# Kernel optimization log

Hardware: AMD Instinct MI355X
Metric: run time of the kernel (lower is better)

Reference implementation:

```python
import jax, jax.numpy as jnp
import numpy as np


def setup_inputs() -> dict:
    key = jax.random.key(0)
    k1, k2, k3 = jax.random.split(key, 3)
    x = jax.random.normal(k1, (8192, 2048), dtype=jnp.float32)
    w = jax.random.normal(k2, (4096, 2048), dtype=jnp.float32) * 0.02  # [out, in]
    b = jax.random.normal(k3, (4096,), dtype=jnp.float32) * 0.01
    return {"x": x, "w": w, "b": b}


def reference(x, w, b):
    # Straight-through binarization: forward uses sign(w), gradient flows as identity.
    binary_w = w + jax.lax.stop_gradient(jnp.sign(w) - w)  # [out, in], values in {-1, 0, 1}
    # F.linear: x @ W^T + b
    return jnp.einsum("ni,oi->no", x, binary_w) + b
```

## Files before the change

kernel.cpp:

```cpp
#include <hip/hip_runtime.h>
#include <hip/hip_bf16.h>
#include <stdint.h>

typedef __bf16 bf16x8 __attribute__((ext_vector_type(8)));
typedef float  f32x16 __attribute__((ext_vector_type(16)));


__device__ __forceinline__ uint32_t rn2_bf16(uint32_t lo, uint32_t hi) {
  uint32_t rlo = (lo + 0x7FFFu + ((lo >> 16) & 1u)) >> 16;
  uint32_t rhi = (hi + 0x7FFFu + ((hi >> 16) & 1u)) >> 16;
  return (rhi << 16) | (rlo & 0xFFFFu);
}

__device__ __forceinline__ uint32_t sign2_bf16(uint32_t lo, uint32_t hi) {
  uint32_t slo = (lo & 0x7FFFFFFFu) ? (0x3F80u | ((lo >> 16) & 0x8000u)) : 0u;
  uint32_t shi = (hi & 0x7FFFFFFFu) ? (0x3F80u | ((hi >> 16) & 0x8000u)) : 0u;
  return (shi << 16) | slo;
}

__device__ __forceinline__ void gl16(const void* g, void* l) {
  __builtin_amdgcn_global_load_lds(
      (const __attribute__((address_space(1))) uint32_t*)g,
      (__attribute__((address_space(3))) uint32_t*)l,
      16, 0, 0);
}


__global__ void prep_frag(const float* __restrict__ x, uint4* __restrict__ xf, int Mx,
                          const float* __restrict__ w, uint4* __restrict__ wf, int Nw,
                          int K) {
  const int kpw = K >> 6;
  const long nxc = ((long)Mx * K) >> 3;
  const long nwc = ((long)Nw * K) >> 3;
  const long stride = (long)gridDim.x * blockDim.x;
  for (long c = (long)blockIdx.x * blockDim.x + threadIdx.x; c < nxc + nwc; c += stride) {
    const bool isX = (c < nxc);
    const float* src = isX ? x : w;
    uint4* dst = isX ? xf : wf;
    const int rows32 = (isX ? Mx : Nw) >> 5;
    const long cc = isX ? c : (c - nxc);

    const int t = (int)(cc & 63);
    const long wv = cc >> 6;
    const int band = (int)(wv / kpw);
    const int kg = (int)(wv % kpw);
    const int row = band * 8 + (t & 7);
    const int k8 = kg * 8 + (t >> 3);

    const int kt = k8 >> 3, ks = (k8 >> 1) & 3, sub = k8 & 1;
    const int mb = row >> 5, r = row & 31;
    const long out16 = ((long)(kt * rows32 + mb) * 4 + ks) * 64 + sub * 32 + r;

    const uint4* s = reinterpret_cast<const uint4*>(src + (long)row * K + k8 * 8);
    uint4 a = s[0], b = s[1];
    uint4 o;
    if (isX) {
      o.x = rn2_bf16(a.x, a.y); o.y = rn2_bf16(a.z, a.w);
      o.z = rn2_bf16(b.x, b.y); o.w = rn2_bf16(b.z, b.w);
    } else {
      o.x = sign2_bf16(a.x, a.y); o.y = sign2_bf16(a.z, a.w);
      o.z = sign2_bf16(b.x, b.y); o.w = sign2_bf16(b.z, b.w);
    }
    dst[out16] = o;
  }
}


#define BARX()  do { __builtin_amdgcn_s_barrier(); \
                     __builtin_amdgcn_sched_barrier(0); } while (0)
#define VM0()   asm volatile("s_waitcnt vmcnt(0)" ::: "memory")
#define VMN8()  asm volatile("s_waitcnt vmcnt(8)" ::: "memory")
#define SGB(m, n) __builtin_amdgcn_sched_group_barrier((m), (n), 0)
#define MF(a, b, c) __builtin_amdgcn_mfma_f32_32x32x16_bf16((a), (b), (c), 0, 0, 0)

#define PIN6() do { \
    SGB(0x100,1); SGB(0x8,1); SGB(0x100,1); SGB(0x8,1); \
    SGB(0x100,1); SGB(0x8,1); SGB(0x100,1); SGB(0x8,1); \
    SGB(0x100,1); SGB(0x8,1); SGB(0x100,1); SGB(0x8,1); \
    SGB(0x8,2); } while (0)
#define PINV() SGB(0x20,4)

__global__ __launch_bounds__(512, 2) void gemm256(
    const uint16_t* __restrict__ Af,
    const uint16_t* __restrict__ Bf,
    const float* __restrict__ bias,
    float* __restrict__ C,
    int M, int N, int K) {
  __shared__ alignas(16) uint8_t L[131072];
  uint8_t* Lb = L;

  const int tid  = threadIdx.x;
  const int lane = tid & 63;
  const int w    = tid >> 6;
  const int wr   = w >> 2;
  const int wc   = w & 3;
  const int l31  = lane & 31;
  const int lhi  = lane >> 5;

  const int nbx = N >> 8;
  const int nwg = nbx * (M >> 8);
  const int bid = blockIdx.x;
  const int swb = (bid & 7) * (nwg >> 3) + (bid >> 3);
  const size_t m0 = (size_t)(swb / nbx) << 8;
  const size_t n0 = (size_t)(swb % nbx) << 8;

  const int NT = K >> 6;
  const size_t ktA = (size_t)(M >> 5) * 4096;
  const size_t ktB = (size_t)(N >> 5) * 4096;
  const char* Abase = (const char*)Af + (m0 >> 5) * 4096;
  const char* Bbase = (const char*)Bf + (n0 >> 5) * 4096;

  const int wB = w << 11;
  const int g0 = wB + lane * 16;
  const int g1 = g0 + 1024;

#define STG(LOFF, SRC) do { \
    gl16((SRC) + g0, Lb + (LOFF) + wB); \
    gl16((SRC) + g1, Lb + (LOFF) + wB + 1024); } while (0)

#define FRA32(d, i, q) (*reinterpret_cast<const bf16x8*>( \
    Lb + (d) * 65536 + wr * 16384 + (i) * 4096 + (q) * 1024 + lane * 16))
#define FRB32(d, j, q) (*reinterpret_cast<const bf16x8*>( \
    Lb + (d) * 65536 + 32768 + wc * 8192 + (j) * 4096 + (q) * 1024 + lane * 16))

  f32x16 acc[4][2] = {};

#define QMRD(CAa, CAb, Ra, Rb, d, q) do { \
    Ra[0] = FRA32(d, 0, q); \
    acc[0][0] = MF(CAa[0], CAb[0], acc[0][0]); \
    Ra[1] = FRA32(d, 1, q); \
    acc[0][1] = MF(CAa[0], CAb[1], acc[0][1]); \
    Ra[2] = FRA32(d, 2, q); \
    acc[1][0] = MF(CAa[1], CAb[0], acc[1][0]); \
    Ra[3] = FRA32(d, 3, q); \
    acc[1][1] = MF(CAa[1], CAb[1], acc[1][1]); \
    Rb[0] = FRB32(d, 0, q); \
    acc[2][0] = MF(CAa[2], CAb[0], acc[2][0]); \
    Rb[1] = FRB32(d, 1, q); \
    acc[2][1] = MF(CAa[2], CAb[1], acc[2][1]); \
    acc[3][0] = MF(CAa[3], CAb[0], acc[3][0]); \
    acc[3][1] = MF(CAa[3], CAb[1], acc[3][1]); \
  } while (0)

  STG(0,      Abase);
  STG(16384,  Abase + 16384);
  STG(32768,  Bbase);
  STG(49152,  Bbase + 16384);
  STG(65536,  Abase + ktA);
  STG(81920,  Abase + ktA + 16384);
  STG(98304,  Bbase + ktB);
  STG(114688, Bbase + ktB + 16384);
  VMN8();
  BARX();

  bf16x8 S0a[4], S0b[2], S1a[4], S1b[2], S2a[4], S2b[2], S3a[4], S3b[2];
#pragma unroll
  for (int i = 0; i < 4; ++i) S0a[i] = FRA32(0, i, 0);
#pragma unroll
  for (int j = 0; j < 2; ++j) S0b[j] = FRB32(0, j, 0);
#pragma unroll
  for (int i = 0; i < 4; ++i) S1a[i] = FRA32(0, i, 1);
#pragma unroll
  for (int j = 0; j < 2; ++j) S1b[j] = FRB32(0, j, 1);

  const int T2 = K >> 7;
  for (int t = 0; t < T2; ++t) {
    const int u2 = 2 * t + 2, u3 = 2 * t + 3;
    const char* A2 = Abase + (size_t)(u2 < NT ? u2 : NT - 1) * ktA;
    const char* B2 = Bbase + (size_t)(u2 < NT ? u2 : NT - 1) * ktB;
    const char* A3 = Abase + (size_t)(u3 < NT ? u3 : NT - 1) * ktA;
    const char* B3 = Bbase + (size_t)(u3 < NT ? u3 : NT - 1) * ktB;

    QMRD(S0a, S0b, S2a, S2b, 0, 2);
    PIN6();
    BARX();

    QMRD(S1a, S1b, S3a, S3b, 0, 3);
    PIN6();
    VM0();
    BARX();

    STG(0, A2);
    STG(16384, A2 + 16384);
    QMRD(S2a, S2b, S0a, S0b, 1, 0);
    PINV(); PIN6();
    BARX();

    STG(32768, B2);
    STG(49152, B2 + 16384);
    QMRD(S3a, S3b, S1a, S1b, 1, 1);
    PINV(); PIN6();
    BARX();

    QMRD(S0a, S0b, S2a, S2b, 1, 2);
    PIN6();
    BARX();

    QMRD(S1a, S1b, S3a, S3b, 1, 3);
    PIN6();
    VM0();
    BARX();

    STG(65536, A3);
    STG(81920, A3 + 16384);
    QMRD(S2a, S2b, S0a, S0b, 0, 0);
    PINV(); PIN6();
    BARX();

    STG(98304, B3);
    STG(114688, B3 + 16384);
    QMRD(S3a, S3b, S1a, S1b, 0, 1);
    PINV(); PIN6();
    BARX();
  }
  VM0();

#pragma unroll
  for (int i = 0; i < 4; ++i) {
#pragma unroll
    for (int j2 = 0; j2 < 2; ++j2) {
      const size_t col = n0 + wc * 64 + j2 * 32 + l31;
      const float bv = bias[col];
      const size_t rbase = m0 + wr * 128 + i * 32 + lhi * 4;
#pragma unroll
      for (int r = 0; r < 16; ++r) {
        const size_t row = rbase + (r & 3) + 8 * (r >> 2);
        C[row * N + col] = acc[i][j2][r] + bv;
      }
    }
  }
}

__global__ void gemm_naive(const float* __restrict__ x, const float* __restrict__ w,
                           const float* __restrict__ b, float* __restrict__ out,
                           int M, int N, int K) {
  int n = blockIdx.x * blockDim.x + threadIdx.x;
  int m = blockIdx.y;
  if (n >= N || m >= M) return;
  float acc = 0.f;
  for (int k = 0; k < K; ++k) {
    float wv = w[(size_t)n * K + k];
    float s = (wv > 0.f) ? 1.f : ((wv < 0.f) ? -1.f : 0.f);
    acc += x[(size_t)m * K + k] * s;
  }
  out[(size_t)m * N + n] = acc + b[n];
}

extern "C" void kernel_launch(void* const* d_in, const int* in_sizes, int n_in,
                              void* d_out, int out_size, void* d_ws, size_t ws_size,
                              hipStream_t stream) {
  const float* x = (const float*)d_in[0];
  const float* w = (const float*)d_in[1];
  const float* b = (const float*)d_in[2];
  float* out = (float*)d_out;

  const int N = in_sizes[2];
  const int K = in_sizes[1] / N;
  const int M = in_sizes[0] / K;

  const size_t need = ((size_t)M * K + (size_t)N * K) * sizeof(uint16_t);
  const bool big_ok = (M % 256 == 0) && (N % 256 == 0) && (K % 256 == 0) &&
                      (((M / 256) * (N / 256)) % 8 == 0) && (ws_size >= need);
  if (!big_ok) {
    hipLaunchKernelGGL(gemm_naive, dim3((N + 255) / 256, M), dim3(256), 0, stream,
                       x, w, b, out, M, N, K);
    return;
  }

  uint16_t* Xf = (uint16_t*)d_ws;
  uint16_t* Wf = Xf + (size_t)M * K;

  hipLaunchKernelGGL(prep_frag, dim3(2048), dim3(256), 0, stream,
                     x, (uint4*)Xf, M, w, (uint4*)Wf, N, K);

  hipLaunchKernelGGL(gemm256, dim3((M / 256) * (N / 256)), dim3(512), 0, stream,
                     Xf, Wf, b, out, M, N, K);
}
```

Baseline: 141.2 us.

## Merge quarter-steps into half-tile steps to halve barriers per K-iteration

Each pipeline phase now covers two k-quarters (16 MFMAs with 12 LDS fragment reads) instead of one. This halves the workgroup barriers in the main loop from eight to four per iteration and issues all A and B global-to-LDS loads of a stage together. The cost is larger fragment register sets (8+4 per buffer), which raises register pressure under the 2-waves-per-SIMD launch bound. Global loads are also issued in bigger bursts, so memory traffic overlaps less evenly with compute.

```diff
diff --git a/kernel.cpp b/kernel.cpp
--- a/kernel.cpp
+++ b/kernel.cpp
@@ -73,12 +73,15 @@
 #define SGB(m, n) __builtin_amdgcn_sched_group_barrier((m), (n), 0)
 #define MF(a, b, c) __builtin_amdgcn_mfma_f32_32x32x16_bf16((a), (b), (c), 0, 0, 0)
 
-#define PIN6() do { \
-    SGB(0x100,1); SGB(0x8,1); SGB(0x100,1); SGB(0x8,1); \
-    SGB(0x100,1); SGB(0x8,1); SGB(0x100,1); SGB(0x8,1); \
-    SGB(0x100,1); SGB(0x8,1); SGB(0x100,1); SGB(0x8,1); \
-    SGB(0x8,2); } while (0)
-#define PINV() SGB(0x20,4)
+#define PIN12() do { \
+    SGB(0x100,1); SGB(0x8,1); SGB(0x100,1); SGB(0x8,1); \
+    SGB(0x100,1); SGB(0x8,1); SGB(0x100,1); SGB(0x8,1); \
+    SGB(0x100,1); SGB(0x8,1); SGB(0x100,1); SGB(0x8,1); \
+    SGB(0x100,1); SGB(0x8,1); SGB(0x100,1); SGB(0x8,1); \
+    SGB(0x100,1); SGB(0x8,1); SGB(0x100,1); SGB(0x8,1); \
+    SGB(0x100,1); SGB(0x8,1); SGB(0x100,1); SGB(0x8,1); \
+    SGB(0x8,4); } while (0)
+#define PINV8() SGB(0x20,8)
 
 __global__ __launch_bounds__(512, 2) void gemm256(
     const uint16_t* __restrict__ Af,
@@ -125,21 +128,23 @@
 
   f32x16 acc[4][2] = {};
 
-#define QMRD(CAa, CAb, Ra, Rb, d, q) do { \
-    Ra[0] = FRA32(d, 0, q); \
-    acc[0][0] = MF(CAa[0], CAb[0], acc[0][0]); \
-    Ra[1] = FRA32(d, 1, q); \
-    acc[0][1] = MF(CAa[0], CAb[1], acc[0][1]); \
-    Ra[2] = FRA32(d, 2, q); \
-    acc[1][0] = MF(CAa[1], CAb[0], acc[1][0]); \
-    Ra[3] = FRA32(d, 3, q); \
-    acc[1][1] = MF(CAa[1], CAb[1], acc[1][1]); \
-    Rb[0] = FRB32(d, 0, q); \
-    acc[2][0] = MF(CAa[2], CAb[0], acc[2][0]); \
-    Rb[1] = FRB32(d, 1, q); \
-    acc[2][1] = MF(CAa[2], CAb[1], acc[2][1]); \
-    acc[3][0] = MF(CAa[3], CAb[0], acc[3][0]); \
-    acc[3][1] = MF(CAa[3], CAb[1], acc[3][1]); \
+#define QMRD2(CA, CB, RA, RB, d, qlo, qhi) do { \
+    RA[0] = FRA32(d, 0, qlo);  acc[0][0] = MF(CA[0], CB[0], acc[0][0]); \
+    RA[1] = FRA32(d, 1, qlo);  acc[0][1] = MF(CA[0], CB[1], acc[0][1]); \
+    RA[2] = FRA32(d, 2, qlo);  acc[1][0] = MF(CA[1], CB[0], acc[1][0]); \
+    RA[3] = FRA32(d, 3, qlo);  acc[1][1] = MF(CA[1], CB[1], acc[1][1]); \
+    RA[4] = FRA32(d, 0, qhi);  acc[2][0] = MF(CA[2], CB[0], acc[2][0]); \
+    RA[5] = FRA32(d, 1, qhi);  acc[2][1] = MF(CA[2], CB[1], acc[2][1]); \
+    RA[6] = FRA32(d, 2, qhi);  acc[3][0] = MF(CA[3], CB[0], acc[3][0]); \
+    RA[7] = FRA32(d, 3, qhi);  acc[3][1] = MF(CA[3], CB[1], acc[3][1]); \
+    RB[0] = FRB32(d, 0, qlo);  acc[0][0] = MF(CA[4], CB[2], acc[0][0]); \
+    RB[1] = FRB32(d, 1, qlo);  acc[0][1] = MF(CA[4], CB[3], acc[0][1]); \
+    RB[2] = FRB32(d, 0, qhi);  acc[1][0] = MF(CA[5], CB[2], acc[1][0]); \
+    RB[3] = FRB32(d, 1, qhi);  acc[1][1] = MF(CA[5], CB[3], acc[1][1]); \
+    acc[2][0] = MF(CA[6], CB[2], acc[2][0]); \
+    acc[2][1] = MF(CA[6], CB[3], acc[2][1]); \
+    acc[3][0] = MF(CA[7], CB[2], acc[3][0]); \
+    acc[3][1] = MF(CA[7], CB[3], acc[3][1]); \
   } while (0)
 
   STG(0,      Abase);
@@ -153,15 +158,11 @@
   VMN8();
   BARX();
 
-  bf16x8 S0a[4], S0b[2], S1a[4], S1b[2], S2a[4], S2b[2], S3a[4], S3b[2];
-#pragma unroll
-  for (int i = 0; i < 4; ++i) S0a[i] = FRA32(0, i, 0);
-#pragma unroll
-  for (int j = 0; j < 2; ++j) S0b[j] = FRB32(0, j, 0);
-#pragma unroll
-  for (int i = 0; i < 4; ++i) S1a[i] = FRA32(0, i, 1);
-#pragma unroll
-  for (int j = 0; j < 2; ++j) S1b[j] = FRB32(0, j, 1);
+  bf16x8 Pa[8], Pb[4], Qa[8], Qb[4];
+#pragma unroll
+  for (int i = 0; i < 4; ++i) { Pa[i] = FRA32(0, i, 0); Pa[4 + i] = FRA32(0, i, 1); }
+#pragma unroll
+  for (int j = 0; j < 2; ++j) { Pb[j] = FRB32(0, j, 0); Pb[2 + j] = FRB32(0, j, 1); }
 
   const int T2 = K >> 7;
   for (int t = 0; t < T2; ++t) {
@@ -171,46 +172,30 @@
     const char* A3 = Abase + (size_t)(u3 < NT ? u3 : NT - 1) * ktA;
     const char* B3 = Bbase + (size_t)(u3 < NT ? u3 : NT - 1) * ktB;
 
-    QMRD(S0a, S0b, S2a, S2b, 0, 2);
-    PIN6();
-    BARX();
-
-    QMRD(S1a, S1b, S3a, S3b, 0, 3);
-    PIN6();
+    QMRD2(Pa, Pb, Qa, Qb, 0, 2, 3);
+    PIN12();
     VM0();
     BARX();
 
-    STG(0, A2);
+    STG(0,     A2);
     STG(16384, A2 + 16384);
-    QMRD(S2a, S2b, S0a, S0b, 1, 0);
-    PINV(); PIN6();
-    BARX();
-
     STG(32768, B2);
     STG(49152, B2 + 16384);
-    QMRD(S3a, S3b, S1a, S1b, 1, 1);
-    PINV(); PIN6();
-    BARX();
-
-    QMRD(S0a, S0b, S2a, S2b, 1, 2);
-    PIN6();
-    BARX();
-
-    QMRD(S1a, S1b, S3a, S3b, 1, 3);
-    PIN6();
+    QMRD2(Qa, Qb, Pa, Pb, 1, 0, 1);
+    PINV8(); PIN12();
+    BARX();
+
+    QMRD2(Pa, Pb, Qa, Qb, 1, 2, 3);
+    PIN12();
     VM0();
     BARX();
 
-    STG(65536, A3);
-    STG(81920, A3 + 16384);
-    QMRD(S2a, S2b, S0a, S0b, 0, 0);
-    PINV(); PIN6();
-    BARX();
-
-    STG(98304, B3);
+    STG(65536,  A3);
+    STG(81920,  A3 + 16384);
+    STG(98304,  B3);
     STG(114688, B3 + 16384);
-    QMRD(S3a, S3b, S1a, S1b, 0, 1);
-    PINV(); PIN6();
+    QMRD2(Qa, Qb, Pa, Pb, 0, 0, 1);
+    PINV8(); PIN12();
     BARX();
   }
   VM0();
```

Result: no change. 141.9 us (+0.5%).
